# Kernel optimization log

Measured on AMD Instinct MI355X. Metric: run time of the kernel, lower is better.

Reference implementation:

```python
import jax, jax.numpy as jnp
import numpy as np

NUM_NODES = 1_000_000
MEM_DIM = 100
TIME_DIM = 100
EDGE_DIM = 172
HIDDEN = 128  # TGN_DECODER_HIDDEN
E = 500_000
IN_DIM = MEM_DIM * 2 + TIME_DIM + EDGE_DIM  # 472


def setup_inputs() -> dict:
    key = jax.random.key(0)
    ks = jax.random.split(key, 12)
    src = jax.random.randint(ks[0], (E,), 0, NUM_NODES)
    dst = jax.random.randint(ks[1], (E,), 0, NUM_NODES)
    t = jax.random.uniform(ks[2], (E,), dtype=jnp.float32) * 1000.0
    edge_attr = jax.random.normal(ks[3], (E, EDGE_DIM), dtype=jnp.float32)
    memory = jax.random.normal(ks[4], (NUM_NODES, MEM_DIM), dtype=jnp.float32)
    last_update = jax.random.uniform(ks[5], (NUM_NODES,), dtype=jnp.float32) * 500.0
    # TimeEncoder: cos(Linear(1, time_dim))
    time_w = jax.random.normal(ks[6], (TIME_DIM,), dtype=jnp.float32) / jnp.sqrt(1.0)
    time_b = jax.random.normal(ks[7], (TIME_DIM,), dtype=jnp.float32)
    # growth head: Linear(IN_DIM, HIDDEN) -> ReLU -> Linear(HIDDEN, 1)
    w1 = jax.random.normal(ks[8], (IN_DIM, HIDDEN), dtype=jnp.float32) / jnp.sqrt(IN_DIM)
    b1 = jnp.zeros((HIDDEN,), dtype=jnp.float32)
    w2 = jax.random.normal(ks[9], (HIDDEN, 1), dtype=jnp.float32) / jnp.sqrt(HIDDEN)
    b2 = jnp.zeros((1,), dtype=jnp.float32)
    return {"src": src, "dst": dst, "t": t, "edge_attr": edge_attr,
            "memory": memory, "last_update": last_update,
            "time_w": time_w, "time_b": time_b,
            "w1": w1, "b1": b1, "w2": w2, "b2": b2}


def reference(src, dst, t, edge_attr, memory, last_update, time_w, time_b, w1, b1, w2, b2):
    # Gather per-node memory rows (irregular indexing)
    src_mem = memory[src]                     # [E, MEM_DIM]
    dst_mem = memory[dst]                     # [E, MEM_DIM]
    delta_t = t - last_update[src]            # [E]
    # TimeEncoder: cos(delta_t * w + b)
    dt_enc = jnp.cos(delta_t[:, None] * time_w[None, :] + time_b[None, :])  # [E, TIME_DIM]
    out = jnp.concatenate([src_mem, dst_mem, dt_enc, edge_attr], axis=1)   # [E, IN_DIM]
    h = jax.nn.relu(out @ w1 + b1)            # [E, HIDDEN]
    growth_score = h @ w2 + b2                # [E, 1]
    return growth_score
```

## Files before the change

### kernel.cpp

```cpp
#include <hip/hip_runtime.h>
#include <hip/hip_bf16.h>
#include <math.h>

#define MEM_DIM  100
#define TIME_DIM 100
#define EDGE_DIM 172
#define HIDDEN   128
#define IN_DIM   472
#define K_PAD    480
#define NCHUNK   15
#define BM       64
#define BK       32

typedef __attribute__((ext_vector_type(8))) short bf16x8;
typedef __attribute__((ext_vector_type(4))) float floatx4;

typedef const __attribute__((address_space(1))) unsigned int* gp_t;
typedef __attribute__((address_space(3))) unsigned int* lp_t;

__global__ void prep_w1(const float* __restrict__ w1, __hip_bfloat16* __restrict__ w1p) {
    int idx = blockIdx.x * 256 + threadIdx.x;
    if (idx >= K_PAD * HIDDEN) return;
    int k = idx >> 7;
    int n = idx & 127;
    float v = (k < IN_DIM) ? w1[k * HIDDEN + n] : 0.0f;
    int c = k >> 5, kl = k & 31, quad = kl >> 3, j = kl & 7;
    int t = n >> 4, r = n & 15;
    int off = ((c * 8 + t) * 64 + quad * 16 + r) * 8 + j;
    w1p[off] = __float2bfloat16(v);
}

__global__ __launch_bounds__(256, 6)
void tgn_mfma(const int* __restrict__ src, const int* __restrict__ dst,
              const float* __restrict__ t, const float* __restrict__ edge_attr,
              const float* __restrict__ memory, const float* __restrict__ last_update,
              const float* __restrict__ time_w, const float* __restrict__ time_b,
              const __hip_bfloat16* __restrict__ w1p, const float* __restrict__ b1,
              const float* __restrict__ w2, const float* __restrict__ b2,
              float* __restrict__ out, int E)
{
    __shared__ __hip_bfloat16 Xs[BM * BK];
    __shared__ __hip_bfloat16 W1s[8 * 64 * 8];
    __shared__ int   s_src[BM];
    __shared__ int   s_dst[BM];
    __shared__ float s_dt[BM];
    __shared__ float s_tw[TIME_DIM], s_tb[TIME_DIM];
    __shared__ float s_b1[HIDDEN], s_w2[HIDDEN];

    const int tid  = threadIdx.x;
    const int e0   = blockIdx.x * BM;
    const int g    = tid >> 6;
    const int lane = tid & 63;
    const int quad = (tid >> 4) & 3;
    const int r    = tid & 15;

    if (tid < BM) {
        int e = e0 + tid; if (e >= E) e = E - 1;
        int s = src[e];
        s_src[tid] = s;
        s_dst[tid] = dst[e];
        s_dt[tid]  = t[e] - last_update[s];
    }
    if (tid < HIDDEN) { s_b1[tid] = b1[tid]; s_w2[tid] = w2[tid]; }
    if (tid < TIME_DIM) { s_tw[tid] = time_w[tid]; s_tb[tid] = time_b[tid]; }
    __syncthreads();

    const int m = g * 16 + r;
    const float* srcrow = memory + (long)s_src[m] * MEM_DIM;
    const float* dstrow = memory + (long)s_dst[m] * MEM_DIM;
    int em = e0 + m; if (em >= E) em = E - 1;
    const float* earow = edge_attr + (long)em * EDGE_DIM;
    const float dt = s_dt[m];

    floatx4 acc[8];
    #pragma unroll
    for (int i = 0; i < 8; ++i) acc[i] = (floatx4){0.f, 0.f, 0.f, 0.f};

    for (int c = 0; c < NCHUNK; ++c) {
        {
            const __hip_bfloat16* w1c = w1p + c * (8 * 64 * 8);
            const __hip_bfloat16* gsrc = w1c + g * 1024 + lane * 8;
            __hip_bfloat16* ldst = W1s + g * 1024;
            __builtin_amdgcn_global_load_lds((gp_t)(const void*)gsrc,
                                             (lp_t)(void*)ldst, 16, 0, 0);
            __builtin_amdgcn_global_load_lds((gp_t)(const void*)(gsrc + 512),
                                             (lp_t)(void*)(ldst + 512), 16, 0, 0);
        }
        {
            const int kb = c * BK + quad * 8;
            float v[8];
            if (kb + 7 < MEM_DIM) {
                float4 lo = *(const float4*)(srcrow + kb);
                float4 hi = *(const float4*)(srcrow + kb + 4);
                v[0]=lo.x; v[1]=lo.y; v[2]=lo.z; v[3]=lo.w;
                v[4]=hi.x; v[5]=hi.y; v[6]=hi.z; v[7]=hi.w;
            } else if (kb >= MEM_DIM && kb + 7 < 2 * MEM_DIM) {
                float4 lo = *(const float4*)(dstrow + kb - MEM_DIM);
                float4 hi = *(const float4*)(dstrow + kb - MEM_DIM + 4);
                v[0]=lo.x; v[1]=lo.y; v[2]=lo.z; v[3]=lo.w;
                v[4]=hi.x; v[5]=hi.y; v[6]=hi.z; v[7]=hi.w;
            } else if (kb >= 200 && kb + 7 < 300) {
                int c0 = kb - 200;
                #pragma unroll
                for (int j = 0; j < 8; ++j)
                    v[j] = cosf(dt * s_tw[c0 + j] + s_tb[c0 + j]);
            } else if (kb >= 300 && kb + 7 < IN_DIM) {
                float4 lo = *(const float4*)(earow + kb - 300);
                float4 hi = *(const float4*)(earow + kb - 300 + 4);
                v[0]=lo.x; v[1]=lo.y; v[2]=lo.z; v[3]=lo.w;
                v[4]=hi.x; v[5]=hi.y; v[6]=hi.z; v[7]=hi.w;
            } else {
                #pragma unroll
                for (int j = 0; j < 8; ++j) {
                    int k = kb + j;
                    float x;
                    if (k < MEM_DIM)          x = srcrow[k];
                    else if (k < 2 * MEM_DIM) x = dstrow[k - MEM_DIM];
                    else if (k < 300)         x = cosf(dt * s_tw[k - 200] + s_tb[k - 200]);
                    else if (k < IN_DIM)      x = earow[k - 300];
                    else                      x = 0.0f;
                    v[j] = x;
                }
            }
            short fr[8];
            #pragma unroll
            for (int j = 0; j < 8; ++j)
                fr[j] = (short)__bfloat16_as_ushort(__float2bfloat16(v[j]));
            ((bf16x8*)Xs)[tid] = *(bf16x8*)fr;
        }
        __syncthreads();

        bf16x8 afrag = ((bf16x8*)Xs)[g * 64 + lane];
        #pragma unroll
        for (int tnum = 0; tnum < 8; ++tnum) {
            bf16x8 bfrag = ((bf16x8*)W1s)[tnum * 64 + lane];
            acc[tnum] = __builtin_amdgcn_mfma_f32_16x16x32_bf16(afrag, bfrag, acc[tnum], 0, 0, 0);
        }
        __syncthreads();
    }

    float part[4] = {0.f, 0.f, 0.f, 0.f};
    #pragma unroll
    for (int tnum = 0; tnum < 8; ++tnum) {
        int n = tnum * 16 + r;
        float b1n = s_b1[n];
        float w2n = s_w2[n];
        #pragma unroll
        for (int reg = 0; reg < 4; ++reg) {
            float h = acc[tnum][reg] + b1n;
            h = h > 0.f ? h : 0.f;
            part[reg] += h * w2n;
        }
    }
    const float b2v = b2[0];
    #pragma unroll
    for (int reg = 0; reg < 4; ++reg) {
        float p = part[reg];
        p += __shfl_xor(p, 1, 64);
        p += __shfl_xor(p, 2, 64);
        p += __shfl_xor(p, 4, 64);
        p += __shfl_xor(p, 8, 64);
        if (r == 0) {
            int e = e0 + g * 16 + quad * 4 + reg;
            if (e < E) out[e] = p + b2v;
        }
    }
}

extern "C" void kernel_launch(void* const* d_in, const int* in_sizes, int n_in,
                              void* d_out, int out_size, void* d_ws, size_t ws_size,
                              hipStream_t stream) {
    const int*   src = (const int*)d_in[0];
    const int*   dst = (const int*)d_in[1];
    const float* t   = (const float*)d_in[2];
    const float* ea  = (const float*)d_in[3];
    const float* mem = (const float*)d_in[4];
    const float* lu  = (const float*)d_in[5];
    const float* tw  = (const float*)d_in[6];
    const float* tb  = (const float*)d_in[7];
    const float* w1  = (const float*)d_in[8];
    const float* b1  = (const float*)d_in[9];
    const float* w2  = (const float*)d_in[10];
    const float* b2  = (const float*)d_in[11];
    float* out = (float*)d_out;
    const int E = in_sizes[0];

    __hip_bfloat16* w1p = (__hip_bfloat16*)d_ws;

    prep_w1<<<(K_PAD * HIDDEN + 255) / 256, 256, 0, stream>>>(w1, w1p);

    int grid = (E + BM - 1) / BM;
    tgn_mfma<<<grid, 256, 0, stream>>>(src, dst, t, ea, mem, lu, tw, tb,
                                       w1p, b1, w2, b2, out, E);
}
```

Baseline: 816.9 us.

## Stage all of W1 in LDS once per block and build A fragments in registers

Each block now has 1024 threads and handles 256 edges. The whole packed bf16 W1 (about 120KB) is loaded into dynamic LDS once at block start, instead of streaming an 8KB chunk per K-step. The A operand is converted straight into registers, since each thread's fragment was its own Xs slot. That removes the Xs staging buffer and both per-chunk __syncthreads, and the chunk loop is fully unrolled so gather loads can be issued early. The cost is lower occupancy: the large LDS footprint likely allows one block per CU. The per-block W1 load also sits on the critical path before compute, which may reduce latency hiding for the random memory-row gathers.

```diff
diff --git a/kernel.cpp b/kernel.cpp
--- a/kernel.cpp
+++ b/kernel.cpp
@@ -9,8 +9,10 @@
 #define IN_DIM   472
 #define K_PAD    480
 #define NCHUNK   15
-#define BM       64
-#define BK       32
+#define BM       256
+#define THREADS  1024
+#define W1_ELEMS (NCHUNK * 8 * 64 * 8)
+#define W1_BYTES (W1_ELEMS * 2)
 
 typedef __attribute__((ext_vector_type(8))) short bf16x8;
 typedef __attribute__((ext_vector_type(4))) float floatx4;
@@ -30,7 +32,7 @@
     w1p[off] = __float2bfloat16(v);
 }
 
-__global__ __launch_bounds__(256, 6)
+__global__ __launch_bounds__(THREADS, 4)
 void tgn_mfma(const int* __restrict__ src, const int* __restrict__ dst,
               const float* __restrict__ t, const float* __restrict__ edge_attr,
               const float* __restrict__ memory, const float* __restrict__ last_update,
@@ -39,13 +41,13 @@
               const float* __restrict__ w2, const float* __restrict__ b2,
               float* __restrict__ out, int E)
 {
-    __shared__ __hip_bfloat16 Xs[BM * BK];
-    __shared__ __hip_bfloat16 W1s[8 * 64 * 8];
+    extern __shared__ __hip_bfloat16 W1s[];
     __shared__ int   s_src[BM];
     __shared__ int   s_dst[BM];
     __shared__ float s_dt[BM];
     __shared__ float s_tw[TIME_DIM], s_tb[TIME_DIM];
     __shared__ float s_b1[HIDDEN], s_w2[HIDDEN];
+    __shared__ float s_out[BM];
 
     const int tid  = threadIdx.x;
     const int e0   = blockIdx.x * BM;
@@ -54,6 +56,15 @@
     const int quad = (tid >> 4) & 3;
     const int r    = tid & 15;
 
+    #pragma unroll
+    for (int i = 0; i < 8; ++i) {
+        int off = i * (THREADS * 16) + tid * 16;
+        if (off < W1_BYTES) {
+            __builtin_amdgcn_global_load_lds(
+                (gp_t)(const void*)((const char*)w1p + off),
+                (lp_t)(void*)((char*)W1s + off), 16, 0, 0);
+        }
+    }
     if (tid < BM) {
         int e = e0 + tid; if (e >= E) e = E - 1;
         int s = src[e];
@@ -76,67 +87,53 @@
     #pragma unroll
     for (int i = 0; i < 8; ++i) acc[i] = (floatx4){0.f, 0.f, 0.f, 0.f};
 
+    #pragma unroll
     for (int c = 0; c < NCHUNK; ++c) {
-        {
-            const __hip_bfloat16* w1c = w1p + c * (8 * 64 * 8);
-            const __hip_bfloat16* gsrc = w1c + g * 1024 + lane * 8;
-            __hip_bfloat16* ldst = W1s + g * 1024;
-            __builtin_amdgcn_global_load_lds((gp_t)(const void*)gsrc,
-                                             (lp_t)(void*)ldst, 16, 0, 0);
-            __builtin_amdgcn_global_load_lds((gp_t)(const void*)(gsrc + 512),
-                                             (lp_t)(void*)(ldst + 512), 16, 0, 0);
-        }
-        {
-            const int kb = c * BK + quad * 8;
-            float v[8];
-            if (kb + 7 < MEM_DIM) {
-                float4 lo = *(const float4*)(srcrow + kb);
-                float4 hi = *(const float4*)(srcrow + kb + 4);
-                v[0]=lo.x; v[1]=lo.y; v[2]=lo.z; v[3]=lo.w;
-                v[4]=hi.x; v[5]=hi.y; v[6]=hi.z; v[7]=hi.w;
-            } else if (kb >= MEM_DIM && kb + 7 < 2 * MEM_DIM) {
-                float4 lo = *(const float4*)(dstrow + kb - MEM_DIM);
-                float4 hi = *(const float4*)(dstrow + kb - MEM_DIM + 4);
-                v[0]=lo.x; v[1]=lo.y; v[2]=lo.z; v[3]=lo.w;
-                v[4]=hi.x; v[5]=hi.y; v[6]=hi.z; v[7]=hi.w;
-            } else if (kb >= 200 && kb + 7 < 300) {
-                int c0 = kb - 200;
-                #pragma unroll
-                for (int j = 0; j < 8; ++j)
-                    v[j] = cosf(dt * s_tw[c0 + j] + s_tb[c0 + j]);
-            } else if (kb >= 300 && kb + 7 < IN_DIM) {
-                float4 lo = *(const float4*)(earow + kb - 300);
-                float4 hi = *(const float4*)(earow + kb - 300 + 4);
-                v[0]=lo.x; v[1]=lo.y; v[2]=lo.z; v[3]=lo.w;
-                v[4]=hi.x; v[5]=hi.y; v[6]=hi.z; v[7]=hi.w;
-            } else {
-                #pragma unroll
-                for (int j = 0; j < 8; ++j) {
-                    int k = kb + j;
-                    float x;
-                    if (k < MEM_DIM)          x = srcrow[k];
-                    else if (k < 2 * MEM_DIM) x = dstrow[k - MEM_DIM];
-                    else if (k < 300)         x = cosf(dt * s_tw[k - 200] + s_tb[k - 200]);
-                    else if (k < IN_DIM)      x = earow[k - 300];
-                    else                      x = 0.0f;
-                    v[j] = x;
-                }
-            }
-            short fr[8];
+        const int kb = c * 32 + quad * 8;
+        float v[8];
+        if (kb + 7 < MEM_DIM) {
+            float4 lo = *(const float4*)(srcrow + kb);
+            float4 hi = *(const float4*)(srcrow + kb + 4);
+            v[0]=lo.x; v[1]=lo.y; v[2]=lo.z; v[3]=lo.w;
+            v[4]=hi.x; v[5]=hi.y; v[6]=hi.z; v[7]=hi.w;
+        } else if (kb >= MEM_DIM && kb + 7 < 2 * MEM_DIM) {
+            float4 lo = *(const float4*)(dstrow + kb - MEM_DIM);
+            float4 hi = *(const float4*)(dstrow + kb - MEM_DIM + 4);
+            v[0]=lo.x; v[1]=lo.y; v[2]=lo.z; v[3]=lo.w;
+            v[4]=hi.x; v[5]=hi.y; v[6]=hi.z; v[7]=hi.w;
+        } else if (kb >= 200 && kb + 7 < 300) {
+            int c0 = kb - 200;
             #pragma unroll
             for (int j = 0; j < 8; ++j)
-                fr[j] = (short)__bfloat16_as_ushort(__float2bfloat16(v[j]));
-            ((bf16x8*)Xs)[tid] = *(bf16x8*)fr;
-        }
-        __syncthreads();
-
-        bf16x8 afrag = ((bf16x8*)Xs)[g * 64 + lane];
+                v[j] = cosf(dt * s_tw[c0 + j] + s_tb[c0 + j]);
+        } else if (kb >= 300 && kb + 7 < IN_DIM) {
+            float4 lo = *(const float4*)(earow + kb - 300);
+            float4 hi = *(const float4*)(earow + kb - 300 + 4);
+            v[0]=lo.x; v[1]=lo.y; v[2]=lo.z; v[3]=lo.w;
+            v[4]=hi.x; v[5]=hi.y; v[6]=hi.z; v[7]=hi.w;
+        } else {
+            #pragma unroll
+            for (int j = 0; j < 8; ++j) {
+                int k = kb + j;
+                float x;
+                if (k < MEM_DIM)          x = srcrow[k];
+                else if (k < 2 * MEM_DIM) x = dstrow[k - MEM_DIM];
+                else if (k < 300)         x = cosf(dt * s_tw[k - 200] + s_tb[k - 200]);
+                else if (k < IN_DIM)      x = earow[k - 300];
+                else                      x = 0.0f;
+                v[j] = x;
+            }
+        }
+        bf16x8 af;
+        #pragma unroll
+        for (int j = 0; j < 8; ++j)
+            af[j] = (short)__bfloat16_as_ushort(__float2bfloat16(v[j]));
+
         #pragma unroll
         for (int tnum = 0; tnum < 8; ++tnum) {
-            bf16x8 bfrag = ((bf16x8*)W1s)[tnum * 64 + lane];
-            acc[tnum] = __builtin_amdgcn_mfma_f32_16x16x32_bf16(afrag, bfrag, acc[tnum], 0, 0, 0);
-        }
-        __syncthreads();
+            bf16x8 bfrag = ((bf16x8*)W1s)[(c * 8 + tnum) * 64 + lane];
+            acc[tnum] = __builtin_amdgcn_mfma_f32_16x16x32_bf16(af, bfrag, acc[tnum], 0, 0, 0);
+        }
     }
 
     float part[4] = {0.f, 0.f, 0.f, 0.f};
@@ -160,10 +157,12 @@
         p += __shfl_xor(p, 2, 64);
         p += __shfl_xor(p, 4, 64);
         p += __shfl_xor(p, 8, 64);
-        if (r == 0) {
-            int e = e0 + g * 16 + quad * 4 + reg;
-            if (e < E) out[e] = p + b2v;
-        }
+        if (r == 0) s_out[g * 16 + quad * 4 + reg] = p + b2v;
+    }
+    __syncthreads();
+    if (tid < BM) {
+        int e = e0 + tid;
+        if (e < E) out[e] = s_out[tid];
     }
 }
 
@@ -187,9 +186,17 @@
 
     __hip_bfloat16* w1p = (__hip_bfloat16*)d_ws;
 
+    static bool attr_set = false;
+    if (!attr_set) {
+        (void)hipFuncSetAttribute(reinterpret_cast<const void*>(tgn_mfma),
+                                  hipFuncAttributeMaxDynamicSharedMemorySize,
+                                  W1_BYTES);
+        attr_set = true;
+    }
+
     prep_w1<<<(K_PAD * HIDDEN + 255) / 256, 256, 0, stream>>>(w1, w1p);
 
     int grid = (E + BM - 1) / BM;
-    tgn_mfma<<<grid, 256, 0, stream>>>(src, dst, t, ea, mem, lu, tw, tb,
-                                       w1p, b1, w2, b2, out, E);
+    tgn_mfma<<<grid, THREADS, W1_BYTES, stream>>>(src, dst, t, ea, mem, lu, tw, tb,
+                                                  w1p, b1, w2, b2, out, E);
 }
```

After: 795.4 us. 2.6% less time.
